# Kernel tuning notes

Measured on AMD Instinct MI355X. Metric: run time of the kernel, lower is better.

The kernel has to match this reference:

```python
import jax, jax.numpy as jnp
import numpy as np

B, C, H, W = 4, 64, 64, 64

def _conv1x1(x, w, b):
    # Conv2d(k=1): y[b,o,h,w] = sum_c x[b,c,h,w]*w[o,c] + b[o]
    return jnp.einsum('bchw,oc->bohw', x, w) + b[None, :, None, None]

def setup_inputs() -> dict:
    key = jax.random.key(0)
    ks = jax.random.split(key, 8)
    s = 1.0 / np.sqrt(C)
    return {
        'v1': jax.random.normal(ks[0], (B, C, H, W), jnp.float32),
        'v2': jax.random.normal(ks[1], (B, C, H, W), jnp.float32),
        'wq': jax.random.normal(ks[2], (C, C), jnp.float32) * s,
        'bq': jax.random.normal(ks[3], (C,), jnp.float32) * 0.01,
        'wk': jax.random.normal(ks[4], (C, C), jnp.float32) * s,
        'bk': jax.random.normal(ks[5], (C,), jnp.float32) * 0.01,
        'wv': jax.random.normal(ks[6], (C, C), jnp.float32) * s,
        'bv': jax.random.normal(ks[7], (C,), jnp.float32) * 0.01,
    }

def reference(v1, v2, wq, bq, wk, bk, wv, bv):
    q = _conv1x1(v1, wq, bq)   # (B,C,H,W)
    k = _conv1x1(v2, wk, bk)
    v = _conv1x1(v2, wv, bv)
    b, c, h, w = q.shape
    n = c * h                   # tokens = C*H, feature dim = W (matches torch view)
    qf = q.reshape(b, n, w)
    kf = k.reshape(b, n, w)
    vf = v.reshape(b, n, w)
    scores = jnp.einsum('bnw,bmw->bnm', qf, kf)   # (B, N, N)
    attn = jax.nn.softmax(scores, axis=-1)
    out = jnp.einsum('bnm,bmw->bnw', attn, vf)
    return out.reshape(v1.shape)
```

## Files before the change

### kernel.cpp

```cpp
#include <hip/hip_runtime.h>


#define Bn 4
#define Cc 64
#define HW 4096
#define Nn 4096
#define Dd 64
#define TS (Bn * Nn * Dd)
#define LOG2E 1.44269504088896340736f

typedef _Float16 f16;
typedef _Float16 f16x8 __attribute__((ext_vector_type(8)));
typedef _Float16 f16x4 __attribute__((ext_vector_type(4)));
typedef __fp16 fp16x2 __attribute__((ext_vector_type(2)));
typedef float f32x4 __attribute__((ext_vector_type(4)));

__device__ __forceinline__ int swz(int row, int col) {
    return row * 64 + (col ^ ((row & 7) << 3));
}

__device__ __forceinline__ void gl_lds16(const f16* g, f16* l) {
    __builtin_amdgcn_global_load_lds(
        (const __attribute__((address_space(1))) unsigned int*)g,
        (__attribute__((address_space(3))) unsigned int*)l, 16, 0, 0);
}

__global__ __launch_bounds__(512) void qkv_conv(
    const float* __restrict__ v1, const float* __restrict__ v2,
    const float* __restrict__ wq, const float* __restrict__ bq,
    const float* __restrict__ wk, const float* __restrict__ bk,
    const float* __restrict__ wv, const float* __restrict__ bv,
    f16* __restrict__ Qh, f16* __restrict__ Kh, f16* __restrict__ Vh)
{
    __shared__ __align__(16) f16 wl[64 * 72];
    __shared__ __align__(16) f16 Xt[64 * 72];
    __shared__ __align__(16) float bl[64];

    const int t    = threadIdx.x;
    const int lane = t & 63, wvi = t >> 6;
    const int g = lane >> 4, c = lane & 15;
    const int b   = blockIdx.y;
    const int blk = blockIdx.x;
    const int z   = blockIdx.z;

    const float* w    = (z == 0) ? wq : (z == 1) ? wk : wv;
    const float* bias = (z == 0) ? bq : (z == 1) ? bk : bv;
    const float* x    = ((z == 0) ? v1 : v2) + (size_t)b * (Cc * HW) + blk * 64;
    f16* dst          = (z == 0) ? Qh : (z == 1) ? Kh : Vh;
    const float scale = (z == 0) ? LOG2E : 1.0f;

    for (int i = t; i < 4096; i += 512)
        wl[(i >> 6) * 72 + (i & 63)] = (f16)(w[i] * scale);
    if (t < 64) bl[t] = bias[t] * scale;
    {
        const int cch = t >> 3, dp0 = (t & 7) * 8;
        float4 x0 = *(const float4*)(x + (size_t)cch * HW + dp0);
        float4 x1 = *(const float4*)(x + (size_t)cch * HW + dp0 + 4);
        Xt[(dp0 + 0) * 72 + cch] = (f16)x0.x;
        Xt[(dp0 + 1) * 72 + cch] = (f16)x0.y;
        Xt[(dp0 + 2) * 72 + cch] = (f16)x0.z;
        Xt[(dp0 + 3) * 72 + cch] = (f16)x0.w;
        Xt[(dp0 + 4) * 72 + cch] = (f16)x1.x;
        Xt[(dp0 + 5) * 72 + cch] = (f16)x1.y;
        Xt[(dp0 + 6) * 72 + cch] = (f16)x1.z;
        Xt[(dp0 + 7) * 72 + cch] = (f16)x1.w;
    }
    __syncthreads();

    const int fn  = wvi & 3;
    const int fo2 = (wvi >> 2) * 2;

    f16x8 xb0 = *(const f16x8*)(Xt + (fn * 16 + c) * 72 + g * 8);
    f16x8 xb1 = *(const f16x8*)(Xt + (fn * 16 + c) * 72 + 32 + g * 8);

    #pragma unroll
    for (int fi = 0; fi < 2; ++fi) {
        const int fo = fo2 + fi;
        f16x8 wa0 = *(const f16x8*)(wl + (fo * 16 + c) * 72 + g * 8);
        f16x8 wa1 = *(const f16x8*)(wl + (fo * 16 + c) * 72 + 32 + g * 8);
        f32x4 acc = *(const f32x4*)(bl + fo * 16 + g * 4);
        acc = __builtin_amdgcn_mfma_f32_16x16x32_f16(wa0, xb0, acc, 0, 0, 0);
        acc = __builtin_amdgcn_mfma_f32_16x16x32_f16(wa1, xb1, acc, 0, 0, 0);
        #pragma unroll
        for (int r = 0; r < 4; ++r) {
            const int o = fo * 16 + g * 4 + r;
            const int n = o * 64 + blk;
            dst[(size_t)b * (Nn * Dd) + (size_t)n * 64 + fn * 16 + c] = (f16)acc[r];
        }
    }
}

__global__ __launch_bounds__(256) void vtrans(const f16* __restrict__ Vh,
                                              f16* __restrict__ Vt)
{
    __shared__ f16 tile[64][72];
    const int t  = threadIdx.x;
    const int n0 = blockIdx.x * 64;
    const int b  = blockIdx.y;
    for (int i = t; i < 4096; i += 256) {
        int r = i >> 6, c = i & 63;
        tile[r][c] = Vh[(size_t)b * (Nn * Dd) + (size_t)(n0 + r) * 64 + c];
    }
    __syncthreads();
    for (int i = t; i < 4096; i += 256) {
        int w = i >> 6, n = i & 63;
        Vt[(size_t)b * (Dd * Nn) + (size_t)w * Nn + n0 + n] = tile[n][w];
    }
}

__global__ __launch_bounds__(512, 4) void attn(
    const f16* __restrict__ Qhg, const f16* __restrict__ Khg,
    const f16* __restrict__ Vtg,
    float* __restrict__ out, f16* __restrict__ Opart, float* __restrict__ lw)
{
    __shared__ __align__(16) f16 KT[2][2][4096];
    __shared__ __align__(16) f16 VT[2][2][4096];

    const int t    = threadIdx.x;
    const int lane = t & 63, wvi = t >> 6;
    const int g = lane >> 4, c = lane & 15;
    const int b  = blockIdx.z;
    const int sp = blockIdx.y;
    const int S  = gridDim.y;
    const int n0 = blockIdx.x * 256;
    const int keysPerSplit = Nn / S;
    const int nPairs = keysPerSplit / 128;
    const int kbase = sp * keysPerSplit;

    const int srow = t >> 3;
    const int gc   = ((t & 7) ^ (srow & 7)) * 8;
    const int ldsoff = (wvi * 8) * 64;

    const f16* Kb = Khg + (size_t)b * (Nn * Dd);
    const f16* Vb = Vtg + (size_t)b * (Dd * Nn);

    f16x8 qbh[2][2];
    #pragma unroll
    for (int qf = 0; qf < 2; ++qf) {
        const int qrow = n0 + wvi * 32 + qf * 16 + c;
        const f16* qhp = Qhg + ((size_t)b * Nn + qrow) * 64;
        #pragma unroll
        for (int ks = 0; ks < 2; ++ks)
            qbh[qf][ks] = *(const f16x8*)(qhp + ks * 32 + g * 8);
    }

    float m_run[2] = {-1e30f, -1e30f}, lpart[2] = {0.f, 0.f};
    f32x4 of[2][4];
    #pragma unroll
    for (int qf = 0; qf < 2; ++qf)
        #pragma unroll
        for (int nf = 0; nf < 4; ++nf)
            #pragma unroll
            for (int r = 0; r < 4; ++r) of[qf][nf][r] = 0.f;

    #pragma unroll
    for (int sub = 0; sub < 2; ++sub) {
        const int k0 = kbase + sub * 64;
        gl_lds16(Kb + (size_t)(k0 + srow) * 64 + gc, &KT[0][sub][ldsoff]);
        gl_lds16(Vb + (size_t)srow * Nn + k0 + gc, &VT[0][sub][ldsoff]);
    }
    __syncthreads();
    int cur = 0;

    for (int pr = 0; pr < nPairs; ++pr) {
        if (pr + 1 < nPairs) {
            const int kp = kbase + (pr + 1) * 128;
            #pragma unroll
            for (int sub = 0; sub < 2; ++sub) {
                const int k0 = kp + sub * 64;
                gl_lds16(Kb + (size_t)(k0 + srow) * 64 + gc, &KT[cur ^ 1][sub][ldsoff]);
                gl_lds16(Vb + (size_t)srow * Nn + k0 + gc, &VT[cur ^ 1][sub][ldsoff]);
            }
        }

        #pragma unroll
        for (int sub = 0; sub < 2; ++sub) {
            const f16* KTc = KT[cur][sub];
            const f16* VTc = VT[cur][sub];

            f32x4 accS[2][4];
            #pragma unroll
            for (int qf = 0; qf < 2; ++qf)
                #pragma unroll
                for (int fm = 0; fm < 4; ++fm)
                    #pragma unroll
                    for (int r = 0; r < 4; ++r) accS[qf][fm][r] = 0.f;
            #pragma unroll
            for (int fm = 0; fm < 4; ++fm) {
                const int key = fm * 16 + c;
                f16x8 kh0 = *(const f16x8*)(KTc + swz(key, g * 8));
                f16x8 kh1 = *(const f16x8*)(KTc + swz(key, 32 + g * 8));
                #pragma unroll
                for (int qf = 0; qf < 2; ++qf) {
                    accS[qf][fm] = __builtin_amdgcn_mfma_f32_16x16x32_f16(kh0, qbh[qf][0], accS[qf][fm], 0, 0, 0);
                    accS[qf][fm] = __builtin_amdgcn_mfma_f32_16x16x32_f16(kh1, qbh[qf][1], accS[qf][fm], 0, 0, 0);
                }
            }

            f16x4 pb[2][4];
            #pragma unroll
            for (int qf = 0; qf < 2; ++qf) {
                float m0 = fmaxf(fmaxf(accS[qf][0][0], accS[qf][0][1]),
                                 fmaxf(accS[qf][0][2], accS[qf][0][3]));
                float m1 = fmaxf(fmaxf(accS[qf][1][0], accS[qf][1][1]),
                                 fmaxf(accS[qf][1][2], accS[qf][1][3]));
                float m2 = fmaxf(fmaxf(accS[qf][2][0], accS[qf][2][1]),
                                 fmaxf(accS[qf][2][2], accS[qf][2][3]));
                float m3 = fmaxf(fmaxf(accS[qf][3][0], accS[qf][3][1]),
                                 fmaxf(accS[qf][3][2], accS[qf][3][3]));
                float tmax = fmaxf(fmaxf(m0, m1), fmaxf(m2, m3));
                tmax = fmaxf(tmax, __shfl_xor(tmax, 16));
                tmax = fmaxf(tmax, __shfl_xor(tmax, 32));
                if (!__all(tmax <= m_run[qf] + 8.f)) {
                    const float mnew = fmaxf(m_run[qf], tmax);
                    const float corr = exp2f(m_run[qf] - mnew);
                    lpart[qf] *= corr;
                    #pragma unroll
                    for (int nf = 0; nf < 4; ++nf)
                        #pragma unroll
                        for (int r = 0; r < 4; ++r) of[qf][nf][r] *= corr;
                    m_run[qf] = mnew;
                }
                float s01 = 0.f, s23 = 0.f;
                #pragma unroll
                for (int fm = 0; fm < 4; ++fm) {
                    #pragma unroll
                    for (int r = 0; r < 4; ++r) {
                        float pp = exp2f(accS[qf][fm][r] - m_run[qf]);
                        accS[qf][fm][r] = pp;
                        if (fm < 2) s01 += pp; else s23 += pp;
                    }
                    union { f16x4 v4; fp16x2 h2[2]; } u;
                    u.h2[0] = __builtin_amdgcn_cvt_pkrtz(accS[qf][fm][0], accS[qf][fm][1]);
                    u.h2[1] = __builtin_amdgcn_cvt_pkrtz(accS[qf][fm][2], accS[qf][fm][3]);
                    pb[qf][fm] = u.v4;
                }
                lpart[qf] += s01 + s23;
            }

            #pragma unroll
            for (int nf = 0; nf < 4; ++nf) {
                #pragma unroll
                for (int fm = 0; fm < 4; ++fm) {
                    f16x4 va = *(const f16x4*)(VTc + swz(nf * 16 + c, fm * 16 + g * 4));
                    of[0][nf] = __builtin_amdgcn_mfma_f32_16x16x16f16(va, pb[0][fm], of[0][nf], 0, 0, 0);
                    of[1][nf] = __builtin_amdgcn_mfma_f32_16x16x16f16(va, pb[1][fm], of[1][nf], 0, 0, 0);
                }
            }
        }

        __syncthreads();
        cur ^= 1;
    }

    if (S == 1) {
        #pragma unroll
        for (int qf = 0; qf < 2; ++qf) {
            float lr = lpart[qf];
            lr += __shfl_xor(lr, 16);
            lr += __shfl_xor(lr, 32);
            const float linv = 1.0f / lr;
            const int n = n0 + wvi * 32 + qf * 16 + c;
            #pragma unroll
            for (int nf = 0; nf < 4; ++nf) {
                float4 o4 = make_float4(of[qf][nf][0] * linv, of[qf][nf][1] * linv,
                                        of[qf][nf][2] * linv, of[qf][nf][3] * linv);
                *(float4*)(out + (((size_t)b * Nn + n) << 6) + nf * 16 + g * 4) = o4;
            }
        }
    } else {
        #pragma unroll
        for (int qf = 0; qf < 2; ++qf) {
            float lr = lpart[qf];
            lr += __shfl_xor(lr, 16);
            lr += __shfl_xor(lr, 32);
            const float linv = 1.0f / lr;
            const int n = n0 + wvi * 32 + qf * 16 + c;
            size_t robase = (((size_t)sp * Bn + b) * Nn + n) << 6;
            #pragma unroll
            for (int nf = 0; nf < 4; ++nf) {
                union { f16x4 v4; fp16x2 h2[2]; } u;
                u.h2[0] = __builtin_amdgcn_cvt_pkrtz(of[qf][nf][0] * linv, of[qf][nf][1] * linv);
                u.h2[1] = __builtin_amdgcn_cvt_pkrtz(of[qf][nf][2] * linv, of[qf][nf][3] * linv);
                *(f16x4*)(Opart + robase + nf * 16 + g * 4) = u.v4;
            }
            if (g == 0) {
                lw[((size_t)sp * Bn + b) * Nn + n] = lr * exp2f(m_run[qf]);
            }
        }
    }
}

__global__ __launch_bounds__(256) void combine(
    const f16* __restrict__ Opart, const float* __restrict__ lw,
    float* __restrict__ out, int S)
{
    const int idx8 = blockIdx.x * 256 + threadIdx.x;
    const int w8 = idx8 & 7;
    const int n  = (idx8 >> 3) & (Nn - 1);
    const int b  = idx8 >> 15;
    float num[8];
    #pragma unroll
    for (int j = 0; j < 8; ++j) num[j] = 0.f;
    float den = 0.f;
    for (int s = 0; s < S; ++s) {
        float a = lw[((size_t)s * Bn + b) * Nn + n];
        f16x8 o8 = *(const f16x8*)(Opart + ((((size_t)s * Bn + b) * Nn + n) << 6) + w8 * 8);
        #pragma unroll
        for (int j = 0; j < 8; ++j) num[j] += a * (float)o8[j];
        den += a;
    }
    const float di = 1.0f / den;
    float* op = out + (((size_t)b * Nn + n) << 6) + w8 * 8;
    float4 lo = make_float4(num[0] * di, num[1] * di, num[2] * di, num[3] * di);
    float4 hi = make_float4(num[4] * di, num[5] * di, num[6] * di, num[7] * di);
    *(float4*)op = lo;
    *(float4*)(op + 4) = hi;
}

extern "C" void kernel_launch(void* const* d_in, const int* in_sizes, int n_in,
                              void* d_out, int out_size, void* d_ws, size_t ws_size,
                              hipStream_t stream)
{
    const float* v1 = (const float*)d_in[0];
    const float* v2 = (const float*)d_in[1];
    const float* wq = (const float*)d_in[2];
    const float* bq = (const float*)d_in[3];
    const float* wk = (const float*)d_in[4];
    const float* bk = (const float*)d_in[5];
    const float* wv = (const float*)d_in[6];
    const float* bv = (const float*)d_in[7];
    float* out = (float*)d_out;

    char* ws = (char*)d_ws;
    const size_t T = (size_t)TS * sizeof(f16);
    f16* Qh = (f16*)(ws + 0 * T);
    f16* Kh = (f16*)(ws + 1 * T);
    f16* Vh = (f16*)(ws + 2 * T);
    f16* Vt = (f16*)(ws + 3 * T);
    const size_t base = 4 * T;
    const size_t opartBytes = (size_t)TS * 2;
    const size_t lwBytes    = (size_t)Bn * Nn * 4;

    int S = 1;
    if      (ws_size >= base + 8 * (opartBytes + lwBytes)) S = 8;
    else if (ws_size >= base + 4 * (opartBytes + lwBytes)) S = 4;
    else if (ws_size >= base + 2 * (opartBytes + lwBytes)) S = 2;

    f16*   Opart = (f16*)(ws + base);
    float* lwp   = (float*)(ws + base + (size_t)S * opartBytes);

    qkv_conv<<<dim3(64, 4, 3), 512, 0, stream>>>(v1, v2, wq, bq, wk, bk, wv, bv,
                                                 Qh, Kh, Vh);
    vtrans<<<dim3(64, 4), 256, 0, stream>>>(Vh, Vt);
    attn<<<dim3(16, S, 4), 512, 0, stream>>>(Qh, Kh, Vt, out, Opart, lwp);
    if (S > 1) {
        combine<<<(Bn * Nn * Dd / 8) / 256, 256, 0, stream>>>(Opart, lwp, out, S);
    }
}
```

Baseline: 63.22 us.

## Halve query tile per block and process full 128-key tile per softmax step

Each wave now owns 16 query rows instead of 32, so a block covers 128 queries and the grid doubles along the query axis. The maximum key-split count drops from 8 to 4. The inner loop now computes scores for all 128 keys of a tile at once, doing one online-softmax max/rescale step per tile instead of one per 64-key half. The aim is fewer rescale and reduction steps and lower register pressure, with parallelism moved from key splits to query blocks. In exchange, each K/V tile loaded into LDS is reused by half as many queries, which raises LDS traffic per MFMA.

```diff
diff --git a/kernel.cpp b/kernel.cpp
--- a/kernel.cpp
+++ b/kernel.cpp
@@ -122,9 +122,9 @@
     const int b  = blockIdx.z;
     const int sp = blockIdx.y;
     const int S  = gridDim.y;
-    const int n0 = blockIdx.x * 256;
+    const int n0 = blockIdx.x * 128;
     const int keysPerSplit = Nn / S;
-    const int nPairs = keysPerSplit / 128;
+    const int nTiles = keysPerSplit / 128;
     const int kbase = sp * keysPerSplit;
 
     const int srow = t >> 3;
@@ -134,24 +134,21 @@
     const f16* Kb = Khg + (size_t)b * (Nn * Dd);
     const f16* Vb = Vtg + (size_t)b * (Dd * Nn);
 
-    f16x8 qbh[2][2];
+    f16x8 qbh[2];
+    {
+        const int qrow = n0 + wvi * 16 + c;
+        const f16* qhp = Qhg + ((size_t)b * Nn + qrow) * 64;
+        #pragma unroll
+        for (int ks = 0; ks < 2; ++ks)
+            qbh[ks] = *(const f16x8*)(qhp + ks * 32 + g * 8);
+    }
+
+    float m_run = -1e30f, lpart = 0.f;
+    f32x4 of[4];
     #pragma unroll
-    for (int qf = 0; qf < 2; ++qf) {
-        const int qrow = n0 + wvi * 32 + qf * 16 + c;
-        const f16* qhp = Qhg + ((size_t)b * Nn + qrow) * 64;
-        #pragma unroll
-        for (int ks = 0; ks < 2; ++ks)
-            qbh[qf][ks] = *(const f16x8*)(qhp + ks * 32 + g * 8);
-    }
-
-    float m_run[2] = {-1e30f, -1e30f}, lpart[2] = {0.f, 0.f};
-    f32x4 of[2][4];
-    #pragma unroll
-    for (int qf = 0; qf < 2; ++qf)
-        #pragma unroll
-        for (int nf = 0; nf < 4; ++nf)
-            #pragma unroll
-            for (int r = 0; r < 4; ++r) of[qf][nf][r] = 0.f;
+    for (int nf = 0; nf < 4; ++nf)
+        #pragma unroll
+        for (int r = 0; r < 4; ++r) of[nf][r] = 0.f;
 
     #pragma unroll
     for (int sub = 0; sub < 2; ++sub) {
@@ -162,9 +159,9 @@
     __syncthreads();
     int cur = 0;
 
-    for (int pr = 0; pr < nPairs; ++pr) {
-        if (pr + 1 < nPairs) {
-            const int kp = kbase + (pr + 1) * 128;
+    for (int kt = 0; kt < nTiles; ++kt) {
+        if (kt + 1 < nTiles) {
+            const int kp = kbase + (kt + 1) * 128;
             #pragma unroll
             for (int sub = 0; sub < 2; ++sub) {
                 const int k0 = kp + sub * 64;
@@ -173,79 +170,67 @@
             }
         }
 
-        #pragma unroll
-        for (int sub = 0; sub < 2; ++sub) {
-            const f16* KTc = KT[cur][sub];
-            const f16* VTc = VT[cur][sub];
-
-            f32x4 accS[2][4];
-            #pragma unroll
-            for (int qf = 0; qf < 2; ++qf)
+        f32x4 accS[8];
+        #pragma unroll
+        for (int fm = 0; fm < 8; ++fm)
+            #pragma unroll
+            for (int r = 0; r < 4; ++r) accS[fm][r] = 0.f;
+        #pragma unroll
+        for (int fm = 0; fm < 8; ++fm) {
+            const f16* KTc = KT[cur][fm >> 2];
+            const int key = (fm & 3) * 16 + c;
+            f16x8 kh0 = *(const f16x8*)(KTc + swz(key, g * 8));
+            f16x8 kh1 = *(const f16x8*)(KTc + swz(key, 32 + g * 8));
+            accS[fm] = __builtin_amdgcn_mfma_f32_16x16x32_f16(kh0, qbh[0], accS[fm], 0, 0, 0);
+            accS[fm] = __builtin_amdgcn_mfma_f32_16x16x32_f16(kh1, qbh[1], accS[fm], 0, 0, 0);
+        }
+
+        f16x4 pb[8];
+        {
+            float mx[8];
+            #pragma unroll
+            for (int fm = 0; fm < 8; ++fm)
+                mx[fm] = fmaxf(fmaxf(accS[fm][0], accS[fm][1]),
+                               fmaxf(accS[fm][2], accS[fm][3]));
+            float t0 = fmaxf(fmaxf(mx[0], mx[1]), fmaxf(mx[2], mx[3]));
+            float t1 = fmaxf(fmaxf(mx[4], mx[5]), fmaxf(mx[6], mx[7]));
+            float tmax = fmaxf(t0, t1);
+            tmax = fmaxf(tmax, __shfl_xor(tmax, 16));
+            tmax = fmaxf(tmax, __shfl_xor(tmax, 32));
+            if (!__all(tmax <= m_run + 8.f)) {
+                const float mnew = fmaxf(m_run, tmax);
+                const float corr = exp2f(m_run - mnew);
+                lpart *= corr;
                 #pragma unroll
-                for (int fm = 0; fm < 4; ++fm)
+                for (int nf = 0; nf < 4; ++nf)
                     #pragma unroll
-                    for (int r = 0; r < 4; ++r) accS[qf][fm][r] = 0.f;
-            #pragma unroll
-            for (int fm = 0; fm < 4; ++fm) {
-                const int key = fm * 16 + c;
-                f16x8 kh0 = *(const f16x8*)(KTc + swz(key, g * 8));
-                f16x8 kh1 = *(const f16x8*)(KTc + swz(key, 32 + g * 8));
-                #pragma unroll
-                for (int qf = 0; qf < 2; ++qf) {
-                    accS[qf][fm] = __builtin_amdgcn_mfma_f32_16x16x32_f16(kh0, qbh[qf][0], accS[qf][fm], 0, 0, 0);
-                    accS[qf][fm] = __builtin_amdgcn_mfma_f32_16x16x32_f16(kh1, qbh[qf][1], accS[qf][fm], 0, 0, 0);
-                }
+                    for (int r = 0; r < 4; ++r) of[nf][r] *= corr;
+                m_run = mnew;
             }
-
-            f16x4 pb[2][4];
-            #pragma unroll
-            for (int qf = 0; qf < 2; ++qf) {
-                float m0 = fmaxf(fmaxf(accS[qf][0][0], accS[qf][0][1]),
-                                 fmaxf(accS[qf][0][2], accS[qf][0][3]));
-                float m1 = fmaxf(fmaxf(accS[qf][1][0], accS[qf][1][1]),
-                                 fmaxf(accS[qf][1][2], accS[qf][1][3]));
-                float m2 = fmaxf(fmaxf(accS[qf][2][0], accS[qf][2][1]),
-                                 fmaxf(accS[qf][2][2], accS[qf][2][3]));
-                float m3 = fmaxf(fmaxf(accS[qf][3][0], accS[qf][3][1]),
-                                 fmaxf(accS[qf][3][2], accS[qf][3][3]));
-                float tmax = fmaxf(fmaxf(m0, m1), fmaxf(m2, m3));
-                tmax = fmaxf(tmax, __shfl_xor(tmax, 16));
-                tmax = fmaxf(tmax, __shfl_xor(tmax, 32));
-                if (!__all(tmax <= m_run[qf] + 8.f)) {
-                    const float mnew = fmaxf(m_run[qf], tmax);
-                    const float corr = exp2f(m_run[qf] - mnew);
-                    lpart[qf] *= corr;
-                    #pragma unroll
-                    for (int nf = 0; nf < 4; ++nf)
-                        #pragma unroll
-                        for (int r = 0; r < 4; ++r) of[qf][nf][r] *= corr;
-                    m_run[qf] = mnew;
-                }
-                float s01 = 0.f, s23 = 0.f;
-                #pragma unroll
-                for (int fm = 0; fm < 4; ++fm) {
-                    #pragma unroll
-                    for (int r = 0; r < 4; ++r) {
-                        float pp = exp2f(accS[qf][fm][r] - m_run[qf]);
-                        accS[qf][fm][r] = pp;
-                        if (fm < 2) s01 += pp; else s23 += pp;
-                    }
-                    union { f16x4 v4; fp16x2 h2[2]; } u;
-                    u.h2[0] = __builtin_amdgcn_cvt_pkrtz(accS[qf][fm][0], accS[qf][fm][1]);
-                    u.h2[1] = __builtin_amdgcn_cvt_pkrtz(accS[qf][fm][2], accS[qf][fm][3]);
-                    pb[qf][fm] = u.v4;
-                }
-                lpart[qf] += s01 + s23;
+            float s0 = 0.f, s1 = 0.f;
+            #pragma unroll
+            for (int fm = 0; fm < 8; ++fm) {
+                float p0 = exp2f(accS[fm][0] - m_run);
+                float p1 = exp2f(accS[fm][1] - m_run);
+                float p2 = exp2f(accS[fm][2] - m_run);
+                float p3 = exp2f(accS[fm][3] - m_run);
+                if (fm < 4) s0 += (p0 + p1) + (p2 + p3);
+                else        s1 += (p0 + p1) + (p2 + p3);
+                union { f16x4 v4; fp16x2 h2[2]; } u;
+                u.h2[0] = __builtin_amdgcn_cvt_pkrtz(p0, p1);
+                u.h2[1] = __builtin_amdgcn_cvt_pkrtz(p2, p3);
+                pb[fm] = u.v4;
             }
-
-            #pragma unroll
-            for (int nf = 0; nf < 4; ++nf) {
-                #pragma unroll
-                for (int fm = 0; fm < 4; ++fm) {
-                    f16x4 va = *(const f16x4*)(VTc + swz(nf * 16 + c, fm * 16 + g * 4));
-                    of[0][nf] = __builtin_amdgcn_mfma_f32_16x16x16f16(va, pb[0][fm], of[0][nf], 0, 0, 0);
-                    of[1][nf] = __builtin_amdgcn_mfma_f32_16x16x16f16(va, pb[1][fm], of[1][nf], 0, 0, 0);
-                }
+            lpart += s0 + s1;
+        }
+
+        #pragma unroll
+        for (int nf = 0; nf < 4; ++nf) {
+            #pragma unroll
+            for (int fm = 0; fm < 8; ++fm) {
+                const f16* VTc = VT[cur][fm >> 2];
+                f16x4 va = *(const f16x4*)(VTc + swz(nf * 16 + c, (fm & 3) * 16 + g * 4));
+                of[nf] = __builtin_amdgcn_mfma_f32_16x16x16f16(va, pb[fm], of[nf], 0, 0, 0);
             }
         }
 
@@ -254,39 +239,33 @@
     }
 
     if (S == 1) {
-        #pragma unroll
-        for (int qf = 0; qf < 2; ++qf) {
-            float lr = lpart[qf];
-            lr += __shfl_xor(lr, 16);
-            lr += __shfl_xor(lr, 32);
-            const float linv = 1.0f / lr;
-            const int n = n0 + wvi * 32 + qf * 16 + c;
-            #pragma unroll
-            for (int nf = 0; nf < 4; ++nf) {
-                float4 o4 = make_float4(of[qf][nf][0] * linv, of[qf][nf][1] * linv,
-                                        of[qf][nf][2] * linv, of[qf][nf][3] * linv);
-                *(float4*)(out + (((size_t)b * Nn + n) << 6) + nf * 16 + g * 4) = o4;
-            }
+        float lr = lpart;
+        lr += __shfl_xor(lr, 16);
+        lr += __shfl_xor(lr, 32);
+        const float linv = 1.0f / lr;
+        const int n = n0 + wvi * 16 + c;
+        #pragma unroll
+        for (int nf = 0; nf < 4; ++nf) {
+            float4 o4 = make_float4(of[nf][0] * linv, of[nf][1] * linv,
+                                    of[nf][2] * linv, of[nf][3] * linv);
+            *(float4*)(out + (((size_t)b * Nn + n) << 6) + nf * 16 + g * 4) = o4;
         }
     } else {
-        #pragma unroll
-        for (int qf = 0; qf < 2; ++qf) {
-            float lr = lpart[qf];
-            lr += __shfl_xor(lr, 16);
-            lr += __shfl_xor(lr, 32);
-            const float linv = 1.0f / lr;
-            const int n = n0 + wvi * 32 + qf * 16 + c;
-            size_t robase = (((size_t)sp * Bn + b) * Nn + n) << 6;
-            #pragma unroll
-            for (int nf = 0; nf < 4; ++nf) {
-                union { f16x4 v4; fp16x2 h2[2]; } u;
-                u.h2[0] = __builtin_amdgcn_cvt_pkrtz(of[qf][nf][0] * linv, of[qf][nf][1] * linv);
-                u.h2[1] = __builtin_amdgcn_cvt_pkrtz(of[qf][nf][2] * linv, of[qf][nf][3] * linv);
-                *(f16x4*)(Opart + robase + nf * 16 + g * 4) = u.v4;
-            }
-            if (g == 0) {
-                lw[((size_t)sp * Bn + b) * Nn + n] = lr * exp2f(m_run[qf]);
-            }
+        float lr = lpart;
+        lr += __shfl_xor(lr, 16);
+        lr += __shfl_xor(lr, 32);
+        const float linv = 1.0f / lr;
+        const int n = n0 + wvi * 16 + c;
+        size_t robase = (((size_t)sp * Bn + b) * Nn + n) << 6;
+        #pragma unroll
+        for (int nf = 0; nf < 4; ++nf) {
+            union { f16x4 v4; fp16x2 h2[2]; } u;
+            u.h2[0] = __builtin_amdgcn_cvt_pkrtz(of[nf][0] * linv, of[nf][1] * linv);
+            u.h2[1] = __builtin_amdgcn_cvt_pkrtz(of[nf][2] * linv, of[nf][3] * linv);
+            *(f16x4*)(Opart + robase + nf * 16 + g * 4) = u.v4;
+        }
+        if (g == 0) {
+            lw[((size_t)sp * Bn + b) * Nn + n] = lr * exp2f(m_run);
         }
     }
 }
@@ -343,8 +322,7 @@
     const size_t lwBytes    = (size_t)Bn * Nn * 4;
 
     int S = 1;
-    if      (ws_size >= base + 8 * (opartBytes + lwBytes)) S = 8;
-    else if (ws_size >= base + 4 * (opartBytes + lwBytes)) S = 4;
+    if      (ws_size >= base + 4 * (opartBytes + lwBytes)) S = 4;
     else if (ws_size >= base + 2 * (opartBytes + lwBytes)) S = 2;
 
     f16*   Opart = (f16*)(ws + base);
@@ -353,7 +331,7 @@
     qkv_conv<<<dim3(64, 4, 3), 512, 0, stream>>>(v1, v2, wq, bq, wk, bk, wv, bv,
                                                  Qh, Kh, Vh);
     vtrans<<<dim3(64, 4), 256, 0, stream>>>(Vh, Vt);
-    attn<<<dim3(16, S, 4), 512, 0, stream>>>(Qh, Kh, Vt, out, Opart, lwp);
+    attn<<<dim3(32, S, 4), 512, 0, stream>>>(Qh, Kh, Vt, out, Opart, lwp);
     if (S > 1) {
         combine<<<(Bn * Nn * Dd / 8) / 256, 256, 0, stream>>>(Opart, lwp, out, S);
     }
```

New measurement: 59.12 us (median of 2 runs). 6.5% less time.
